# Kernel tuning notes

Hardware: AMD Instinct MI355X
Metric: run time of the kernel (lower is better)

## Reference

```python
import jax, jax.numpy as jnp
import numpy as np

N_NODES = 50000
N_EDGES = 600000
D = 128
HIDDEN = 128
OUT = 1


def setup_inputs() -> dict:
    key = jax.random.key(0)
    ks = jax.random.split(key, 6)
    z = jax.random.normal(ks[0], (N_NODES, D), dtype=jnp.float32)
    e = jax.random.randint(ks[1], (2, N_EDGES), 0, N_NODES, dtype=jnp.int64)
    # Linear weights in [in, out] layout; scaled like torch default init
    W1 = jax.random.normal(ks[2], (2 * D, HIDDEN), dtype=jnp.float32) / np.sqrt(2 * D)
    b1 = jax.random.normal(ks[3], (HIDDEN,), dtype=jnp.float32) / np.sqrt(2 * D)
    W2 = jax.random.normal(ks[4], (HIDDEN, OUT), dtype=jnp.float32) / np.sqrt(HIDDEN)
    b2 = jax.random.normal(ks[5], (OUT,), dtype=jnp.float32) / np.sqrt(HIDDEN)
    return {"z": z, "e": e, "W1": W1, "b1": b1, "W2": W2, "b2": b2}


def reference(z, e, W1, b1, W2, b2):
    x_i = z[e[0]]                      # [E, D] gather source nodes
    x_j = z[e[1]]                      # [E, D] gather target nodes
    x = jnp.concatenate([x_i, x_j], axis=1)  # [E, 2D]
    h = jax.nn.relu(x @ W1 + b1)       # [E, HIDDEN]
    out = h @ W2 + b2                  # [E, OUT]
    return jax.nn.sigmoid(out).squeeze()  # [E]
```

## Files before the change

### kernel.cpp

```cpp
#include <hip/hip_runtime.h>


#define DD 128

typedef __attribute__((ext_vector_type(8))) short short8;
typedef __attribute__((ext_vector_type(4))) float floatx4;

static __device__ __forceinline__ unsigned short f2bf(float f) {
  unsigned int u = __builtin_bit_cast(unsigned int, f);
  u += 0x7fffu + ((u >> 16) & 1u);
  return (unsigned short)(u >> 16);
}
static __device__ __forceinline__ float bflo(unsigned int u) {
  return __builtin_bit_cast(float, u << 16);
}
static __device__ __forceinline__ float bfhi(unsigned int u) {
  return __builtin_bit_cast(float, u & 0xffff0000u);
}

__global__ __launch_bounds__(256) void wt_build(
    const float* __restrict__ W1, unsigned short* __restrict__ Wt) {
  const int g = blockIdx.x * 256 + threadIdx.x;
  const int c = g >> 5;
  const int kq = (g & 31) * 4;
  const float* src = (c < 128) ? (W1 + c) : (W1 + 128 * 128 + (c - 128));
  ushort4 o;
  o.x = f2bf(src[(size_t)(kq + 0) * 128]);
  o.y = f2bf(src[(size_t)(kq + 1) * 128]);
  o.z = f2bf(src[(size_t)(kq + 2) * 128]);
  o.w = f2bf(src[(size_t)(kq + 3) * 128]);
  *(ushort4*)&Wt[c * 128 + kq] = o;
}

__global__ __launch_bounds__(512, 4) void node_mfma(
    const float* __restrict__ z, const unsigned short* __restrict__ Wt,
    const float* __restrict__ b1, unsigned short* __restrict__ gi,
    unsigned short* __restrict__ gj, int n_nodes) {
  __shared__ __align__(16) unsigned short zb[64 * 136];
  const int tid = threadIdx.x;
  const int nb = blockIdx.x * 64;

#pragma unroll
  for (int i = 0; i < 4; ++i) {
    int q = tid + i * 512;
    int nl = q >> 5;
    int node = nb + nl; if (node >= n_nodes) node = n_nodes - 1;
    float4 v = ((const float4*)z)[(size_t)node * 32 + (q & 31)];
    ushort4 o;
    o.x = f2bf(v.x); o.y = f2bf(v.y); o.z = f2bf(v.z); o.w = f2bf(v.w);
    *(ushort4*)&zb[nl * 136 + (q & 31) * 4] = o;
  }

  const int w = tid >> 6, lane = tid & 63;
  const int l15 = lane & 15, quad = lane >> 4;

  short8 a[2][4];
#pragma unroll
  for (int tt = 0; tt < 2; ++tt) {
    const unsigned short* wrow =
        Wt + (size_t)((w * 2 + tt) * 16 + l15) * 128 + quad * 8;
#pragma unroll
    for (int s = 0; s < 4; ++s) a[tt][s] = *(const short8*)(wrow + s * 32);
  }

  floatx4 acc[2][4];
#pragma unroll
  for (int tt = 0; tt < 2; ++tt) {
    floatx4 bias = {0.f, 0.f, 0.f, 0.f};
    if (w < 4) {
      float4 b4 = *(const float4*)&b1[(w * 2 + tt) * 16 + quad * 4];
      bias[0] = b4.x; bias[1] = b4.y; bias[2] = b4.z; bias[3] = b4.w;
    }
#pragma unroll
    for (int nt = 0; nt < 4; ++nt) acc[tt][nt] = bias;
  }

  __syncthreads();

#pragma unroll
  for (int nt = 0; nt < 4; ++nt) {
    short8 bz[4];
#pragma unroll
    for (int s = 0; s < 4; ++s)
      bz[s] = *(const short8*)&zb[(nt * 16 + l15) * 136 + s * 32 + quad * 8];
#pragma unroll
    for (int tt = 0; tt < 2; ++tt)
#pragma unroll
      for (int s = 0; s < 4; ++s)
        acc[tt][nt] = __builtin_amdgcn_mfma_f32_16x16x32_bf16(
            a[tt][s], bz[s], acc[tt][nt], 0, 0, 0);
  }

  __syncthreads();
#pragma unroll
  for (int half = 0; half < 2; ++half) {
    if ((w >> 2) == half) {
      const int cbase = (w & 3) * 32;
#pragma unroll
      for (int nt = 0; nt < 4; ++nt) {
        const int row = (nt * 16 + l15) * 136;
#pragma unroll
        for (int tt = 0; tt < 2; ++tt) {
          const int c = cbase + tt * 16 + quad * 4;
          ushort4 o;
          o.x = f2bf(acc[tt][nt][0]); o.y = f2bf(acc[tt][nt][1]);
          o.z = f2bf(acc[tt][nt][2]); o.w = f2bf(acc[tt][nt][3]);
          *(ushort4*)&zb[row + c] = o;
        }
      }
    }
    __syncthreads();
    unsigned short* dst = half ? gj : gi;
#pragma unroll
    for (int it = 0; it < 2; ++it) {
      const int u = tid * 8 + it * 4096;
      const int n = u >> 7, c = u & 127;
      const int node = nb + n;
      ushort4 v0 = *(const ushort4*)&zb[n * 136 + c];
      ushort4 v1 = *(const ushort4*)&zb[n * 136 + c + 4];
      if (node < n_nodes) {
        ushort4* gp = (ushort4*)&dst[(size_t)node * 128 + c];
        gp[0] = v0;
        gp[1] = v1;
      }
    }
    __syncthreads();
  }
}

static __device__ __forceinline__ float dot8(uint4 a, uint4 b, float4 w0, float4 w1) {
  float s;
  s = fmaxf(bflo(a.x) + bflo(b.x), 0.f) * w0.x;
  s = fmaf(fmaxf(bfhi(a.x) + bfhi(b.x), 0.f), w0.y, s);
  s = fmaf(fmaxf(bflo(a.y) + bflo(b.y), 0.f), w0.z, s);
  s = fmaf(fmaxf(bfhi(a.y) + bfhi(b.y), 0.f), w0.w, s);
  s = fmaf(fmaxf(bflo(a.z) + bflo(b.z), 0.f), w1.x, s);
  s = fmaf(fmaxf(bfhi(a.z) + bfhi(b.z), 0.f), w1.y, s);
  s = fmaf(fmaxf(bflo(a.w) + bflo(b.w), 0.f), w1.z, s);
  s = fmaf(fmaxf(bfhi(a.w) + bfhi(b.w), 0.f), w1.w, s);
  return s;
}

__global__ __launch_bounds__(256) void edge_mlp(
    const int* __restrict__ e, const unsigned short* __restrict__ gi,
    const unsigned short* __restrict__ gj, const float* __restrict__ W2,
    const float* __restrict__ b2, float* __restrict__ out, int E) {
  const int p = threadIdx.x & 7;
  const float4* wv = (const float4*)W2;
  const float4 w0 = wv[p * 2],      w1 = wv[p * 2 + 1];
  const float4 w2 = wv[16 + p * 2], w3 = wv[16 + p * 2 + 1];
  const float bias2 = b2[0];

  const int stride = gridDim.x * 32;
  for (int edge = blockIdx.x * 32 + (threadIdx.x >> 3); edge < E; edge += stride) {
    const int i = e[edge];
    const int j = e[E + edge];
    const uint4* pi = (const uint4*)(gi + (size_t)i * 128);
    const uint4* pj = (const uint4*)(gj + (size_t)j * 128);
    uint4 a0 = pi[p], a1 = pi[8 + p];
    uint4 c0 = pj[p], c1 = pj[8 + p];
    float acc = dot8(a0, c0, w0, w1) + dot8(a1, c1, w2, w3);
    acc += __shfl_xor(acc, 1);
    acc += __shfl_xor(acc, 2);
    acc += __shfl_xor(acc, 4);
    if (p == 0) {
      float x = acc + bias2;
      out[edge] = 1.f / (1.f + __expf(-x));
    }
  }
}

__global__ __launch_bounds__(256) void edge_direct(
    const int* __restrict__ e, const float* __restrict__ z,
    const float* __restrict__ W1, const float* __restrict__ b1,
    const float* __restrict__ W2, const float* __restrict__ b2,
    float* __restrict__ out, int E) {
  const int lane = threadIdx.x & 63;
  const int edge = (int)((blockIdx.x * 256u + threadIdx.x) >> 6);
  if (edge >= E) return;
  const int i = e[edge], j = e[E + edge];
  const float* zi = z + (size_t)i * 128;
  const float* zj = z + (size_t)j * 128;
  const int c0 = lane * 2;
  float h0 = b1[c0], h1 = b1[c0 + 1];
  for (int k = 0; k < 128; ++k) {
    float a = zi[k], b = zj[k];
    float2 wt = *(const float2*)&W1[(size_t)k * 128 + c0];
    float2 wb = *(const float2*)&W1[(size_t)(128 + k) * 128 + c0];
    h0 = fmaf(a, wt.x, h0); h1 = fmaf(a, wt.y, h1);
    h0 = fmaf(b, wb.x, h0); h1 = fmaf(b, wb.y, h1);
  }
  float s = fmaxf(h0, 0.f) * W2[c0] + fmaxf(h1, 0.f) * W2[c0 + 1];
#pragma unroll
  for (int off = 1; off < 64; off <<= 1) s += __shfl_xor(s, off);
  if (lane == 0) out[edge] = 1.f / (1.f + __expf(-(s + b2[0])));
}

extern "C" void kernel_launch(void* const* d_in, const int* in_sizes, int n_in,
                              void* d_out, int out_size, void* d_ws, size_t ws_size,
                              hipStream_t stream) {
  const float* z  = (const float*)d_in[0];
  const int*   e  = (const int*)d_in[1];
  const float* W1 = (const float*)d_in[2];
  const float* b1 = (const float*)d_in[3];
  const float* W2 = (const float*)d_in[4];
  const float* b2 = (const float*)d_in[5];
  float* out = (float*)d_out;
  const int n_nodes = in_sizes[0] / DD;
  const int E = in_sizes[1] / 2;

  const size_t g_bytes = (size_t)n_nodes * DD * sizeof(unsigned short);
  const size_t wt_bytes = 256 * 128 * sizeof(unsigned short);

  if (ws_size >= 2 * g_bytes + wt_bytes && n_nodes > 0) {
    unsigned short* gi = (unsigned short*)d_ws;
    unsigned short* gj = (unsigned short*)((char*)d_ws + g_bytes);
    unsigned short* Wt = (unsigned short*)((char*)d_ws + 2 * g_bytes);
    wt_build<<<32, 256, 0, stream>>>(W1, Wt);
    node_mfma<<<(n_nodes + 63) / 64, 512, 0, stream>>>(z, Wt, b1, gi, gj,
                                                       n_nodes);
    edge_mlp<<<2048, 256, 0, stream>>>(e, gi, gj, W2, b2, out, E);
  } else {
    edge_direct<<<(E + 3) / 4, 256, 0, stream>>>(e, z, W1, b1, W2, b2, out, E);
  }
}
```

Baseline: 129.8 us.

## Make node_mfma persistent with double-buffered prefetch of next node tile

The node projection kernel now runs a grid-stride loop over 64-node tiles on a capped grid. Each block loads its weight fragments and bias once, then prefetches the next tile's z rows into registers while running MFMAs on the current tile, and stores them to a second shared buffer at the end of the iteration. The aim is to amortise weight loads and hide global load latency behind compute. The cost is extra registers and shared memory per block, and a smaller grid that may expose less parallelism, since only about two tiles run per block.

```diff
diff --git a/kernel.cpp b/kernel.cpp
--- a/kernel.cpp
+++ b/kernel.cpp
@@ -36,95 +36,158 @@
     const float* __restrict__ z, const unsigned short* __restrict__ Wt,
     const float* __restrict__ b1, unsigned short* __restrict__ gi,
     unsigned short* __restrict__ gj, int n_nodes) {
-  __shared__ __align__(16) unsigned short zb[64 * 136];
+  __shared__ __align__(16) unsigned short zb[2][64 * 136];
   const int tid = threadIdx.x;
-  const int nb = blockIdx.x * 64;
+  const int w = tid >> 6, lane = tid & 63;
+  const int l15 = lane & 15, quad = lane >> 4;
+  const int ntiles = (n_nodes + 63) >> 6;
+
+  short8 a[2][4];
+#pragma unroll
+  for (int tt = 0; tt < 2; ++tt) {
+    const unsigned short* wrow =
+        Wt + (size_t)((w * 2 + tt) * 16 + l15) * 128 + quad * 8;
+#pragma unroll
+    for (int s = 0; s < 4; ++s) a[tt][s] = *(const short8*)(wrow + s * 32);
+  }
+  floatx4 biasv[2];
+#pragma unroll
+  for (int tt = 0; tt < 2; ++tt) {
+    floatx4 b = {0.f, 0.f, 0.f, 0.f};
+    if (w < 4) {
+      float4 b4 = *(const float4*)&b1[(w * 2 + tt) * 16 + quad * 4];
+      b[0] = b4.x; b[1] = b4.y; b[2] = b4.z; b[3] = b4.w;
+    }
+    biasv[tt] = b;
+  }
+
+  int tile = blockIdx.x;
+  if (tile >= ntiles) return;
 
 #pragma unroll
   for (int i = 0; i < 4; ++i) {
     int q = tid + i * 512;
     int nl = q >> 5;
-    int node = nb + nl; if (node >= n_nodes) node = n_nodes - 1;
+    int node = tile * 64 + nl; if (node >= n_nodes) node = n_nodes - 1;
     float4 v = ((const float4*)z)[(size_t)node * 32 + (q & 31)];
     ushort4 o;
     o.x = f2bf(v.x); o.y = f2bf(v.y); o.z = f2bf(v.z); o.w = f2bf(v.w);
-    *(ushort4*)&zb[nl * 136 + (q & 31) * 4] = o;
-  }
-
-  const int w = tid >> 6, lane = tid & 63;
-  const int l15 = lane & 15, quad = lane >> 4;
-
-  short8 a[2][4];
-#pragma unroll
-  for (int tt = 0; tt < 2; ++tt) {
-    const unsigned short* wrow =
-        Wt + (size_t)((w * 2 + tt) * 16 + l15) * 128 + quad * 8;
-#pragma unroll
-    for (int s = 0; s < 4; ++s) a[tt][s] = *(const short8*)(wrow + s * 32);
-  }
-
-  floatx4 acc[2][4];
-#pragma unroll
-  for (int tt = 0; tt < 2; ++tt) {
-    floatx4 bias = {0.f, 0.f, 0.f, 0.f};
-    if (w < 4) {
-      float4 b4 = *(const float4*)&b1[(w * 2 + tt) * 16 + quad * 4];
-      bias[0] = b4.x; bias[1] = b4.y; bias[2] = b4.z; bias[3] = b4.w;
-    }
-#pragma unroll
-    for (int nt = 0; nt < 4; ++nt) acc[tt][nt] = bias;
-  }
-
+    *(ushort4*)&zb[0][nl * 136 + (q & 31) * 4] = o;
+  }
   __syncthreads();
 
-#pragma unroll
-  for (int nt = 0; nt < 4; ++nt) {
-    short8 bz[4];
-#pragma unroll
-    for (int s = 0; s < 4; ++s)
-      bz[s] = *(const short8*)&zb[(nt * 16 + l15) * 136 + s * 32 + quad * 8];
+  int cur = 0;
+  for (; tile < ntiles; tile += gridDim.x) {
+    const int nxt_tile = tile + gridDim.x;
+    const bool has_nxt = nxt_tile < ntiles;
+
+    float4 v0, v1, v2, v3;
+    if (has_nxt) {
+      {
+        int q = tid;          int nl = q >> 5;
+        int node = nxt_tile * 64 + nl; if (node >= n_nodes) node = n_nodes - 1;
+        v0 = ((const float4*)z)[(size_t)node * 32 + (q & 31)];
+      }
+      {
+        int q = tid + 512;    int nl = q >> 5;
+        int node = nxt_tile * 64 + nl; if (node >= n_nodes) node = n_nodes - 1;
+        v1 = ((const float4*)z)[(size_t)node * 32 + (q & 31)];
+      }
+      {
+        int q = tid + 1024;   int nl = q >> 5;
+        int node = nxt_tile * 64 + nl; if (node >= n_nodes) node = n_nodes - 1;
+        v2 = ((const float4*)z)[(size_t)node * 32 + (q & 31)];
+      }
+      {
+        int q = tid + 1536;   int nl = q >> 5;
+        int node = nxt_tile * 64 + nl; if (node >= n_nodes) node = n_nodes - 1;
+        v3 = ((const float4*)z)[(size_t)node * 32 + (q & 31)];
+      }
+    }
+
+    floatx4 acc[2][4];
 #pragma unroll
     for (int tt = 0; tt < 2; ++tt)
 #pragma unroll
+      for (int nt = 0; nt < 4; ++nt) acc[tt][nt] = biasv[tt];
+
+#pragma unroll
+    for (int nt = 0; nt < 4; ++nt) {
+      short8 bz[4];
+#pragma unroll
       for (int s = 0; s < 4; ++s)
-        acc[tt][nt] = __builtin_amdgcn_mfma_f32_16x16x32_bf16(
-            a[tt][s], bz[s], acc[tt][nt], 0, 0, 0);
-  }
-
-  __syncthreads();
-#pragma unroll
-  for (int half = 0; half < 2; ++half) {
-    if ((w >> 2) == half) {
-      const int cbase = (w & 3) * 32;
-#pragma unroll
-      for (int nt = 0; nt < 4; ++nt) {
-        const int row = (nt * 16 + l15) * 136;
-#pragma unroll
-        for (int tt = 0; tt < 2; ++tt) {
-          const int c = cbase + tt * 16 + quad * 4;
-          ushort4 o;
-          o.x = f2bf(acc[tt][nt][0]); o.y = f2bf(acc[tt][nt][1]);
-          o.z = f2bf(acc[tt][nt][2]); o.w = f2bf(acc[tt][nt][3]);
-          *(ushort4*)&zb[row + c] = o;
+        bz[s] = *(const short8*)&zb[cur][(nt * 16 + l15) * 136 + s * 32 + quad * 8];
+#pragma unroll
+      for (int tt = 0; tt < 2; ++tt)
+#pragma unroll
+        for (int s = 0; s < 4; ++s)
+          acc[tt][nt] = __builtin_amdgcn_mfma_f32_16x16x32_bf16(
+              a[tt][s], bz[s], acc[tt][nt], 0, 0, 0);
+    }
+
+    __syncthreads();
+
+    const int nb = tile * 64;
+#pragma unroll
+    for (int half = 0; half < 2; ++half) {
+      if ((w >> 2) == half) {
+        const int cbase = (w & 3) * 32;
+#pragma unroll
+        for (int nt = 0; nt < 4; ++nt) {
+          const int row = (nt * 16 + l15) * 136;
+#pragma unroll
+          for (int tt = 0; tt < 2; ++tt) {
+            const int c = cbase + tt * 16 + quad * 4;
+            ushort4 o;
+            o.x = f2bf(acc[tt][nt][0]); o.y = f2bf(acc[tt][nt][1]);
+            o.z = f2bf(acc[tt][nt][2]); o.w = f2bf(acc[tt][nt][3]);
+            *(ushort4*)&zb[cur][row + c] = o;
+          }
         }
       }
+      __syncthreads();
+      unsigned short* dst = half ? gj : gi;
+#pragma unroll
+      for (int it = 0; it < 2; ++it) {
+        const int u = tid * 8 + it * 4096;
+        const int n = u >> 7, c = u & 127;
+        const int node = nb + n;
+        ushort4 s0 = *(const ushort4*)&zb[cur][n * 136 + c];
+        ushort4 s1 = *(const ushort4*)&zb[cur][n * 136 + c + 4];
+        if (node < n_nodes) {
+          ushort4* gp = (ushort4*)&dst[(size_t)node * 128 + c];
+          gp[0] = s0;
+          gp[1] = s1;
+        }
+      }
+      __syncthreads();
+    }
+
+    if (has_nxt) {
+      const int nxt = cur ^ 1;
+      {
+        int q = tid;        int nl = q >> 5;
+        ushort4 o; o.x = f2bf(v0.x); o.y = f2bf(v0.y); o.z = f2bf(v0.z); o.w = f2bf(v0.w);
+        *(ushort4*)&zb[nxt][nl * 136 + (q & 31) * 4] = o;
+      }
+      {
+        int q = tid + 512;  int nl = q >> 5;
+        ushort4 o; o.x = f2bf(v1.x); o.y = f2bf(v1.y); o.z = f2bf(v1.z); o.w = f2bf(v1.w);
+        *(ushort4*)&zb[nxt][nl * 136 + (q & 31) * 4] = o;
+      }
+      {
+        int q = tid + 1024; int nl = q >> 5;
+        ushort4 o; o.x = f2bf(v2.x); o.y = f2bf(v2.y); o.z = f2bf(v2.z); o.w = f2bf(v2.w);
+        *(ushort4*)&zb[nxt][nl * 136 + (q & 31) * 4] = o;
+      }
+      {
+        int q = tid + 1536; int nl = q >> 5;
+        ushort4 o; o.x = f2bf(v3.x); o.y = f2bf(v3.y); o.z = f2bf(v3.z); o.w = f2bf(v3.w);
+        *(ushort4*)&zb[nxt][nl * 136 + (q & 31) * 4] = o;
+      }
     }
     __syncthreads();
-    unsigned short* dst = half ? gj : gi;
-#pragma unroll
-    for (int it = 0; it < 2; ++it) {
-      const int u = tid * 8 + it * 4096;
-      const int n = u >> 7, c = u & 127;
-      const int node = nb + n;
-      ushort4 v0 = *(const ushort4*)&zb[n * 136 + c];
-      ushort4 v1 = *(const ushort4*)&zb[n * 136 + c + 4];
-      if (node < n_nodes) {
-        ushort4* gp = (ushort4*)&dst[(size_t)node * 128 + c];
-        gp[0] = v0;
-        gp[1] = v1;
-      }
-    }
-    __syncthreads();
+    cur ^= 1;
   }
 }
 
@@ -216,9 +279,11 @@
     unsigned short* gi = (unsigned short*)d_ws;
     unsigned short* gj = (unsigned short*)((char*)d_ws + g_bytes);
     unsigned short* Wt = (unsigned short*)((char*)d_ws + 2 * g_bytes);
+    const int ntiles = (n_nodes + 63) / 64;
+    int ngrid = (ntiles + 1) / 2;
+    if (ngrid > 512) ngrid = 512;
     wt_build<<<32, 256, 0, stream>>>(W1, Wt);
-    node_mfma<<<(n_nodes + 63) / 64, 512, 0, stream>>>(z, Wt, b1, gi, gj,
-                                                       n_nodes);
+    node_mfma<<<ngrid, 512, 0, stream>>>(z, Wt, b1, gi, gj, n_nodes);
     edge_mlp<<<2048, 256, 0, stream>>>(e, gi, gj, W2, b2, out, E);
   } else {
     edge_direct<<<(E + 3) / 4, 256, 0, stream>>>(e, z, W1, b1, W2, b2, out, E);
```

New measurement: 141.9 us. +9.4%, slower.

## Quantize per-node projections to int8 with per-row scales for edge gather

Applied to the files above, without the earlier changes.

The per-node hidden projections are now stored as int8 with one float scale per node (absmax per row) instead of bf16. The edge kernel gathers half as many bytes per edge and dequantizes in registers before the relu and dot with W2. This targets the random-gather bandwidth of the edge stage, at the cost of extra quantization work in the node kernel, extra scale loads, and added numerical error.

```diff
diff --git a/kernel.cpp b/kernel.cpp
--- a/kernel.cpp
+++ b/kernel.cpp
@@ -11,11 +11,8 @@
   u += 0x7fffu + ((u >> 16) & 1u);
   return (unsigned short)(u >> 16);
 }
-static __device__ __forceinline__ float bflo(unsigned int u) {
-  return __builtin_bit_cast(float, u << 16);
-}
-static __device__ __forceinline__ float bfhi(unsigned int u) {
-  return __builtin_bit_cast(float, u & 0xffff0000u);
+static __device__ __forceinline__ float bf2f(unsigned short u) {
+  return __builtin_bit_cast(float, (unsigned int)u << 16);
 }
 
 __global__ __launch_bounds__(256) void wt_build(
@@ -34,8 +31,9 @@
 
 __global__ __launch_bounds__(512, 4) void node_mfma(
     const float* __restrict__ z, const unsigned short* __restrict__ Wt,
-    const float* __restrict__ b1, unsigned short* __restrict__ gi,
-    unsigned short* __restrict__ gj, int n_nodes) {
+    const float* __restrict__ b1, signed char* __restrict__ gqi,
+    signed char* __restrict__ gqj, float* __restrict__ sci,
+    float* __restrict__ scj, int n_nodes) {
   __shared__ __align__(16) unsigned short zb[64 * 136];
   const int tid = threadIdx.x;
   const int nb = blockIdx.x * 64;
@@ -110,62 +108,87 @@
       }
     }
     __syncthreads();
-    unsigned short* dst = half ? gj : gi;
-#pragma unroll
-    for (int it = 0; it < 2; ++it) {
-      const int u = tid * 8 + it * 4096;
-      const int n = u >> 7, c = u & 127;
-      const int node = nb + n;
-      ushort4 v0 = *(const ushort4*)&zb[n * 136 + c];
-      ushort4 v1 = *(const ushort4*)&zb[n * 136 + c + 4];
+    {
+      const int nl = tid >> 3, p8 = tid & 7;
+      const int node = nb + nl;
+      const unsigned short* rowp = &zb[nl * 136 + p8 * 16];
+      ushort4 u0 = *(const ushort4*)(rowp);
+      ushort4 u1 = *(const ushort4*)(rowp + 4);
+      ushort4 u2 = *(const ushort4*)(rowp + 8);
+      ushort4 u3 = *(const ushort4*)(rowp + 12);
+      float f[16];
+      f[0] = bf2f(u0.x); f[1] = bf2f(u0.y); f[2] = bf2f(u0.z); f[3] = bf2f(u0.w);
+      f[4] = bf2f(u1.x); f[5] = bf2f(u1.y); f[6] = bf2f(u1.z); f[7] = bf2f(u1.w);
+      f[8] = bf2f(u2.x); f[9] = bf2f(u2.y); f[10] = bf2f(u2.z); f[11] = bf2f(u2.w);
+      f[12] = bf2f(u3.x); f[13] = bf2f(u3.y); f[14] = bf2f(u3.z); f[15] = bf2f(u3.w);
+      float am = 0.f;
+#pragma unroll
+      for (int k = 0; k < 16; ++k) am = fmaxf(am, fabsf(f[k]));
+      am = fmaxf(am, __shfl_xor(am, 1));
+      am = fmaxf(am, __shfl_xor(am, 2));
+      am = fmaxf(am, __shfl_xor(am, 4));
+      const float inv = (am > 0.f) ? 127.f / am : 0.f;
+      unsigned int wd[4];
+#pragma unroll
+      for (int k2 = 0; k2 < 4; ++k2) {
+        unsigned int v = 0;
+#pragma unroll
+        for (int b = 0; b < 4; ++b) {
+          const int q = (int)rintf(f[k2 * 4 + b] * inv);
+          v |= ((unsigned int)(q & 0xff)) << (8 * b);
+        }
+        wd[k2] = v;
+      }
       if (node < n_nodes) {
-        ushort4* gp = (ushort4*)&dst[(size_t)node * 128 + c];
-        gp[0] = v0;
-        gp[1] = v1;
+        signed char* dq = half ? gqj : gqi;
+        uint4 pk; pk.x = wd[0]; pk.y = wd[1]; pk.z = wd[2]; pk.w = wd[3];
+        ((uint4*)(dq + (size_t)node * 128))[p8] = pk;
+        if (p8 == 0) (half ? scj : sci)[node] = am * (1.f / 127.f);
       }
     }
     __syncthreads();
   }
 }
 
-static __device__ __forceinline__ float dot8(uint4 a, uint4 b, float4 w0, float4 w1) {
-  float s;
-  s = fmaxf(bflo(a.x) + bflo(b.x), 0.f) * w0.x;
-  s = fmaf(fmaxf(bfhi(a.x) + bfhi(b.x), 0.f), w0.y, s);
-  s = fmaf(fmaxf(bflo(a.y) + bflo(b.y), 0.f), w0.z, s);
-  s = fmaf(fmaxf(bfhi(a.y) + bfhi(b.y), 0.f), w0.w, s);
-  s = fmaf(fmaxf(bflo(a.z) + bflo(b.z), 0.f), w1.x, s);
-  s = fmaf(fmaxf(bfhi(a.z) + bfhi(b.z), 0.f), w1.y, s);
-  s = fmaf(fmaxf(bflo(a.w) + bflo(b.w), 0.f), w1.z, s);
-  s = fmaf(fmaxf(bfhi(a.w) + bfhi(b.w), 0.f), w1.w, s);
-  return s;
-}
-
-__global__ __launch_bounds__(256) void edge_mlp(
-    const int* __restrict__ e, const unsigned short* __restrict__ gi,
-    const unsigned short* __restrict__ gj, const float* __restrict__ W2,
+__global__ __launch_bounds__(256) void edge_mlp_q(
+    const int* __restrict__ e, const signed char* __restrict__ gqi,
+    const signed char* __restrict__ gqj, const float* __restrict__ sci,
+    const float* __restrict__ scj, const float* __restrict__ W2,
     const float* __restrict__ b2, float* __restrict__ out, int E) {
   const int p = threadIdx.x & 7;
   const float4* wv = (const float4*)W2;
-  const float4 w0 = wv[p * 2],      w1 = wv[p * 2 + 1];
-  const float4 w2 = wv[16 + p * 2], w3 = wv[16 + p * 2 + 1];
+  float4 W[4];
+#pragma unroll
+  for (int k = 0; k < 4; ++k) W[k] = wv[p * 4 + k];
   const float bias2 = b2[0];
 
   const int stride = gridDim.x * 32;
   for (int edge = blockIdx.x * 32 + (threadIdx.x >> 3); edge < E; edge += stride) {
     const int i = e[edge];
     const int j = e[E + edge];
-    const uint4* pi = (const uint4*)(gi + (size_t)i * 128);
-    const uint4* pj = (const uint4*)(gj + (size_t)j * 128);
-    uint4 a0 = pi[p], a1 = pi[8 + p];
-    uint4 c0 = pj[p], c1 = pj[8 + p];
-    float acc = dot8(a0, c0, w0, w1) + dot8(a1, c1, w2, w3);
+    const float si = sci[i];
+    const float sj = scj[j];
+    const uint4 qa = ((const uint4*)(gqi + (size_t)i * 128))[p];
+    const uint4 qb = ((const uint4*)(gqj + (size_t)j * 128))[p];
+    const unsigned int ua[4] = {qa.x, qa.y, qa.z, qa.w};
+    const unsigned int ub[4] = {qb.x, qb.y, qb.z, qb.w};
+    float acc = 0.f;
+#pragma unroll
+    for (int k = 0; k < 4; ++k) {
+      const float wk[4] = {W[k].x, W[k].y, W[k].z, W[k].w};
+#pragma unroll
+      for (int b = 0; b < 4; ++b) {
+        const float af = (float)(int)(signed char)(ua[k] >> (8 * b));
+        const float bf = (float)(int)(signed char)(ub[k] >> (8 * b));
+        const float h = fmaf(si, af, sj * bf);
+        acc = fmaf(fmaxf(h, 0.f), wk[b], acc);
+      }
+    }
     acc += __shfl_xor(acc, 1);
     acc += __shfl_xor(acc, 2);
     acc += __shfl_xor(acc, 4);
     if (p == 0) {
-      float x = acc + bias2;
-      out[edge] = 1.f / (1.f + __expf(-x));
+      out[edge] = 1.f / (1.f + __expf(-(acc + bias2)));
     }
   }
 }
@@ -209,17 +232,22 @@
   const int n_nodes = in_sizes[0] / DD;
   const int E = in_sizes[1] / 2;
 
-  const size_t g_bytes = (size_t)n_nodes * DD * sizeof(unsigned short);
+  const size_t gq_bytes = (size_t)n_nodes * DD;
+  const size_t sc_bytes = (size_t)n_nodes * sizeof(float);
   const size_t wt_bytes = 256 * 128 * sizeof(unsigned short);
-
-  if (ws_size >= 2 * g_bytes + wt_bytes && n_nodes > 0) {
-    unsigned short* gi = (unsigned short*)d_ws;
-    unsigned short* gj = (unsigned short*)((char*)d_ws + g_bytes);
-    unsigned short* Wt = (unsigned short*)((char*)d_ws + 2 * g_bytes);
+  const size_t need = 2 * gq_bytes + 2 * sc_bytes + wt_bytes;
+
+  if (ws_size >= need && n_nodes > 0) {
+    signed char* gqi = (signed char*)d_ws;
+    signed char* gqj = gqi + gq_bytes;
+    float* sci = (float*)((char*)d_ws + 2 * gq_bytes);
+    float* scj = (float*)((char*)d_ws + 2 * gq_bytes + sc_bytes);
+    unsigned short* Wt =
+        (unsigned short*)((char*)d_ws + 2 * gq_bytes + 2 * sc_bytes);
     wt_build<<<32, 256, 0, stream>>>(W1, Wt);
-    node_mfma<<<(n_nodes + 63) / 64, 512, 0, stream>>>(z, Wt, b1, gi, gj,
-                                                       n_nodes);
-    edge_mlp<<<2048, 256, 0, stream>>>(e, gi, gj, W2, b2, out, E);
+    node_mfma<<<(n_nodes + 63) / 64, 512, 0, stream>>>(z, Wt, b1, gqi, gqj,
+                                                       sci, scj, n_nodes);
+    edge_mlp_q<<<2048, 256, 0, stream>>>(e, gqi, gqj, sci, scj, W2, b2, out, E);
   } else {
     edge_direct<<<(E + 3) / 4, 256, 0, stream>>>(e, z, W1, b1, W2, b2, out, E);
   }
```

After: 114.7 us. -11.6%, faster.
